# Kernel optimization log

Hardware: AMD Instinct MI355X
Metric: run time of the kernel (lower is better)

The kernel has to match this reference:

```python
import jax, jax.numpy as jnp
import numpy as np

B, L, D_MODEL, N_HEADS, M = 1, 2048, 512, 8, 128
D_HEAD = D_MODEL // N_HEADS
KERNEL_EPS = 1e-4
DENOM_EPS = 1e-6


def setup_inputs() -> dict:
    key = jax.random.key(0)
    ks = jax.random.split(key, 12)
    s = 0.02  # weight init scale
    return {
        "query": jax.random.normal(ks[0], (B, L, D_MODEL), jnp.float32),
        "key": jax.random.normal(ks[1], (B, L, D_MODEL), jnp.float32),
        "value": jax.random.normal(ks[2], (B, L, D_MODEL), jnp.float32),
        "Wq": jax.random.normal(ks[3], (D_MODEL, D_MODEL), jnp.float32) * s,
        "bq": jnp.zeros((D_MODEL,), jnp.float32),
        "Wk": jax.random.normal(ks[4], (D_MODEL, D_MODEL), jnp.float32) * s,
        "bk": jnp.zeros((D_MODEL,), jnp.float32),
        "Wv": jax.random.normal(ks[5], (D_MODEL, D_MODEL), jnp.float32) * s,
        "bv": jnp.zeros((D_MODEL,), jnp.float32),
        "Wo": jax.random.normal(ks[6], (D_MODEL, D_MODEL), jnp.float32) * s,
        "bo": jnp.zeros((D_MODEL,), jnp.float32),
        # FAVOR+ random feature matrix (d_head, m); treated as a fixed buffer
        "random_features": jax.random.normal(ks[7], (D_HEAD, M), jnp.float32),
    }


def reference(query, key, value, Wq, bq, Wk, bk, Wv, bv, Wo, bo, random_features):
    b, l, _ = query.shape

    def proj_split(x, W, bias):
        # nn.Linear: x @ W.T + b, then split heads -> (b, h, l, d_head)
        y = x @ W.T + bias
        return y.reshape(b, l, N_HEADS, D_HEAD).transpose(0, 2, 1, 3)

    q = proj_split(query, Wq, bq)
    k = proj_split(key, Wk, bk)
    v = proj_split(value, Wv, bv)

    # --- get_projected_queries_and_keys ('exp' kernel) ---
    scale = D_MODEL ** -0.25
    q = q * scale
    k = k * scale
    proj_q = q @ random_features  # (b, h, l, m)
    proj_k = k @ random_features
    h_q = -0.5 * jnp.sum(q * q, axis=-1, keepdims=True)  # (b, h, l, 1)
    h_k = -0.5 * jnp.sum(k * k, axis=-1, keepdims=True)
    # argmax over a size-1 last dim -> stabilizer is h_q itself (faithful to source)
    q_stab = h_q
    k_stab = jnp.max(h_k)  # global max, scalar
    nc = M ** -0.5
    q_prime = nc * (jnp.exp(h_q + (proj_q - q_stab)) + KERNEL_EPS)  # (b, h, l, m)
    k_prime = nc * (jnp.exp(h_k + (proj_k - k_stab)) + KERNEL_EPS)

    # --- causal numerator: per-head cumsum of k' (x) v outer products ---
    head_outs = []
    for h in range(N_HEADS):
        outer = jnp.einsum('blm,bld->blmd', k_prime[:, h], v[:, h])  # (b, l, m, d)
        prefix = jnp.cumsum(outer, axis=1)
        head_outs.append(jnp.einsum('blmd,blm->bld', prefix, q_prime[:, h]))
    numerator = jnp.stack(head_outs, axis=1)  # (b, h, l, d)

    # --- causal denominator: q' . cumsum(k') ---
    denom = jnp.einsum('bhlm,bhlm->bhl', q_prime, jnp.cumsum(k_prime, axis=2))
    context = numerator / (denom[..., None] + DENOM_EPS)

    # unshape and output projection
    context = context.transpose(0, 2, 1, 3).reshape(b, l, D_MODEL)
    return context @ Wo.T + bo
```

## Files before the change

### kernel.cpp

```cpp
#include <hip/hip_runtime.h>
#include <math.h>


#define L       2048
#define DMODEL  512
#define NH      8
#define DH      64
#define M       128
#define CT      64
#define NC      (L/CT)
#define KEPS    1e-4f
#define DEPS    1e-6f
#define SCALE   0.2102241038134286f
#define NCONST  0.08838834764831845f

#define OFF_VB     0
#define OFF_QPB    524288
#define OFF_KPB    1572864
#define OFF_SSB    2621440
#define OFF_SSZ    3670016
#define OFF_CTX    3702784
#define OFF_END    4227072

typedef short bf16x8 __attribute__((ext_vector_type(8)));
typedef float f32x4  __attribute__((ext_vector_type(4)));
typedef __bf16 bf2_t __attribute__((ext_vector_type(2)));
typedef unsigned short ushort_t;

__device__ __forceinline__ ushort_t f2bf(float f) {
    union { __bf16 b; ushort_t u; } cv;
    cv.b = (__bf16)f;
    return cv.u;
}
__device__ __forceinline__ float bf2f(ushort_t u) {
    return __uint_as_float(((unsigned)u) << 16);
}
__device__ __forceinline__ unsigned pack2(float a, float b) {
    bf2_t v;
    v.x = (__bf16)a;
    v.y = (__bf16)b;
    union { bf2_t v; unsigned u; } cv;
    cv.v = v;
    return cv.u;
}

__global__ __launch_bounds__(256) void qkvp_kernel(
    const float* __restrict__ xq, const float* __restrict__ xk, const float* __restrict__ xv,
    const float* __restrict__ Wq, const float* __restrict__ bq,
    const float* __restrict__ Wk, const float* __restrict__ bk,
    const float* __restrict__ Wv, const float* __restrict__ bv,
    const float* __restrict__ RF,
    ushort_t* __restrict__ Vb, ushort_t* __restrict__ QPb, ushort_t* __restrict__ KPb)
{
    __shared__ __align__(16) char smem[24832];
    __shared__ ushort_t Qt[64 * 136];
    __shared__ float ssq[128];
    uint4* As8 = (uint4*)smem;
    uint4* Bs8 = (uint4*)(smem + 520 * 16);
    ushort_t* RFTs = (ushort_t*)smem;

    const int tid  = threadIdx.x;
    const int lane = tid & 63;
    const int wave = tid >> 6;
    const int quad = lane >> 4;
    const int l15  = lane & 15;
    const int z = blockIdx.z;
    const int isK = (z == 1);
    const int row0 = blockIdx.x * 64;
    const int col0 = blockIdx.y * 128;

    const float* X; const float* W; const float* bias;
    if (z == 0)      { X = xq; W = Wq; bias = bq; }
    else if (z == 1) { X = xk; W = Wk; bias = bk; }
    else             { X = xv; W = Wv; bias = bv; }

    f32x4 acc[4][2];
    const f32x4 z4 = {0.f, 0.f, 0.f, 0.f};
    #pragma unroll
    for (int i = 0; i < 4; ++i) { acc[i][0] = z4; acc[i][1] = z4; }

    uint4 ra[2], rb[4];
    auto loadA = [&](int ck) {
        #pragma unroll
        for (int it = 0; it < 2; ++it) {
            int t = tid + it * 256;
            int row = t >> 3, k8 = t & 7;
            const float4* gp = (const float4*)&X[(row0 + row) * DMODEL + ck * 64 + k8 * 8];
            float4 v0 = gp[0], v1 = gp[1];
            ra[it] = make_uint4(pack2(v0.x, v0.y), pack2(v0.z, v0.w),
                                pack2(v1.x, v1.y), pack2(v1.z, v1.w));
        }
    };
    auto loadB = [&](int ck) {
        #pragma unroll
        for (int it = 0; it < 4; ++it) {
            int t = tid + it * 256;
            int col = t >> 3, k8 = t & 7;
            const float4* gp = (const float4*)&W[(col0 + col) * DMODEL + ck * 64 + k8 * 8];
            float4 v0 = gp[0], v1 = gp[1];
            rb[it] = make_uint4(pack2(v0.x, v0.y), pack2(v0.z, v0.w),
                                pack2(v1.x, v1.y), pack2(v1.z, v1.w));
        }
    };

    loadA(0); loadB(0);
    const int wn = wave;
    for (int ck = 0; ck < 8; ++ck) {
        __syncthreads();
        #pragma unroll
        for (int it = 0; it < 2; ++it) {
            int t = tid + it * 256;
            As8[(t & 7) * 65 + (t >> 3)] = ra[it];
        }
        #pragma unroll
        for (int it = 0; it < 4; ++it) {
            int t = tid + it * 256;
            Bs8[(t & 7) * 129 + (t >> 3)] = rb[it];
        }
        __syncthreads();
        if (ck < 7) { loadA(ck + 1); loadB(ck + 1); }
        const bf16x8* Av = (const bf16x8*)As8;
        const bf16x8* Bv = (const bf16x8*)Bs8;
        #pragma unroll
        for (int kc = 0; kc < 2; ++kc) {
            const int k8 = kc * 4 + quad;
            bf16x8 af[4], bfr[2];
            #pragma unroll
            for (int i = 0; i < 4; ++i) af[i] = Av[k8 * 65 + i * 16 + l15];
            #pragma unroll
            for (int j = 0; j < 2; ++j) bfr[j] = Bv[k8 * 129 + wn * 32 + j * 16 + l15];
            #pragma unroll
            for (int i = 0; i < 4; ++i)
                #pragma unroll
                for (int j = 0; j < 2; ++j)
                    acc[i][j] = __builtin_amdgcn_mfma_f32_16x16x32_bf16(af[i], bfr[j], acc[i][j], 0, 0, 0);
        }
    }

    if (z == 2) {
        #pragma unroll
        for (int i = 0; i < 4; ++i)
            #pragma unroll
            for (int j = 0; j < 2; ++j) {
                int c = col0 + wn * 32 + j * 16 + l15;
                float bv_ = bias[c];
                #pragma unroll
                for (int reg = 0; reg < 4; ++reg) {
                    int r = row0 + i * 16 + quad * 4 + reg;
                    Vb[r * DMODEL + c] = f2bf(acc[i][j][reg] + bv_);
                }
            }
        return;
    }

    #pragma unroll
    for (int i = 0; i < 4; ++i)
        #pragma unroll
        for (int j = 0; j < 2; ++j) {
            int c = wn * 32 + j * 16 + l15;
            float bv_ = bias[col0 + c];
            #pragma unroll
            for (int reg = 0; reg < 4; ++reg) {
                int r = i * 16 + quad * 4 + reg;
                Qt[r * 136 + c] = f2bf(acc[i][j][reg] + bv_);
            }
        }
    __syncthreads();

    {
        int m = tid & 127, half = tid >> 7;
        #pragma unroll
        for (int j = 0; j < 32; ++j) {
            int d = half * 32 + j;
            RFTs[m * 72 + d] = f2bf(SCALE * RF[d * M + m]);
        }
    }
    if (isK && tid < 128) {
        int hh = tid >> 6, row = tid & 63;
        float s = 0.f;
        #pragma unroll
        for (int d = 0; d < DH; ++d) {
            float v = bf2f(Qt[row * 136 + hh * 64 + d]);
            s += v * v;
        }
        ssq[tid] = s;
    }
    __syncthreads();

    const int hh = wave >> 1, mh = wave & 1;
    const float s2h = 0.5f * SCALE * SCALE;
    f32x4 pac[4][4];
    #pragma unroll
    for (int i = 0; i < 4; ++i)
        #pragma unroll
        for (int j = 0; j < 4; ++j) pac[i][j] = z4;
    #pragma unroll
    for (int kc = 0; kc < 2; ++kc) {
        bf16x8 af[4], bfr[4];
        #pragma unroll
        for (int i = 0; i < 4; ++i)
            af[i] = *(const bf16x8*)&Qt[(i * 16 + l15) * 136 + hh * 64 + kc * 32 + quad * 8];
        #pragma unroll
        for (int j = 0; j < 4; ++j)
            bfr[j] = *(const bf16x8*)&RFTs[(mh * 64 + j * 16 + l15) * 72 + kc * 32 + quad * 8];
        #pragma unroll
        for (int i = 0; i < 4; ++i)
            #pragma unroll
            for (int j = 0; j < 4; ++j)
                pac[i][j] = __builtin_amdgcn_mfma_f32_16x16x32_bf16(af[i], bfr[j], pac[i][j], 0, 0, 0);
    }

    ushort_t* dst = isK ? KPb : QPb;
    const int hgl = blockIdx.y * 2 + hh;
    #pragma unroll
    for (int i = 0; i < 4; ++i)
        #pragma unroll
        for (int reg = 0; reg < 4; ++reg) {
            int row = i * 16 + quad * 4 + reg;
            float off = isK ? (-s2h * ssq[hh * 64 + row]) : 0.f;
            #pragma unroll
            for (int j = 0; j < 4; ++j) {
                int m = mh * 64 + j * 16 + l15;
                float p = pac[i][j][reg] + off;
                dst[((long)hgl * L + row0 + row) * M + m] = f2bf(NCONST * (__expf(p) + KEPS));
            }
        }
}

__global__ __launch_bounds__(256) void out_gemm_kernel(
    const ushort_t* __restrict__ ctxb, const float* __restrict__ Wo,
    const float* __restrict__ bo, float* __restrict__ out)
{
    __shared__ uint4 As8[8 * 33];
    __shared__ uint4 Bs8[8 * 129];
    const int tid  = threadIdx.x;
    const int lane = tid & 63;
    const int wn   = tid >> 6;
    const int quad = lane >> 4;
    const int l15  = lane & 15;
    const int row0 = blockIdx.x * 32;
    const int col0 = blockIdx.y * 128;

    f32x4 acc[2][2];
    const f32x4 z4 = {0.f, 0.f, 0.f, 0.f};
    acc[0][0] = z4; acc[0][1] = z4; acc[1][0] = z4; acc[1][1] = z4;

    uint4 ra, rb[4];
    auto loadA = [&](int ck) {
        int row = tid >> 3, k8 = tid & 7;
        ra = *(const uint4*)&ctxb[(row0 + row) * DMODEL + ck * 64 + k8 * 8];
    };
    auto loadB = [&](int ck) {
        #pragma unroll
        for (int it = 0; it < 4; ++it) {
            int t = tid + it * 256;
            int col = t >> 3, k8 = t & 7;
            const float4* gp = (const float4*)&Wo[(col0 + col) * DMODEL + ck * 64 + k8 * 8];
            float4 v0 = gp[0], v1 = gp[1];
            rb[it] = make_uint4(pack2(v0.x, v0.y), pack2(v0.z, v0.w),
                                pack2(v1.x, v1.y), pack2(v1.z, v1.w));
        }
    };

    loadA(0); loadB(0);
    for (int ck = 0; ck < 8; ++ck) {
        __syncthreads();
        As8[(tid & 7) * 33 + (tid >> 3)] = ra;
        #pragma unroll
        for (int it = 0; it < 4; ++it) {
            int t = tid + it * 256;
            Bs8[(t & 7) * 129 + (t >> 3)] = rb[it];
        }
        __syncthreads();
        if (ck < 7) { loadA(ck + 1); loadB(ck + 1); }
        const bf16x8* Av = (const bf16x8*)As8;
        const bf16x8* Bv = (const bf16x8*)Bs8;
        #pragma unroll
        for (int kc = 0; kc < 2; ++kc) {
            const int k8 = kc * 4 + quad;
            bf16x8 af[2], bfr[2];
            af[0] = Av[k8 * 33 + l15];
            af[1] = Av[k8 * 33 + 16 + l15];
            #pragma unroll
            for (int j = 0; j < 2; ++j) bfr[j] = Bv[k8 * 129 + wn * 32 + j * 16 + l15];
            #pragma unroll
            for (int i = 0; i < 2; ++i)
                #pragma unroll
                for (int j = 0; j < 2; ++j)
                    acc[i][j] = __builtin_amdgcn_mfma_f32_16x16x32_bf16(af[i], bfr[j], acc[i][j], 0, 0, 0);
        }
    }
    #pragma unroll
    for (int i = 0; i < 2; ++i)
        #pragma unroll
        for (int j = 0; j < 2; ++j) {
            int c = col0 + wn * 32 + j * 16 + l15;
            float bv_ = bo[c];
            #pragma unroll
            for (int reg = 0; reg < 4; ++reg) {
                int r = row0 + i * 16 + quad * 4 + reg;
                out[r * DMODEL + c] = acc[i][j][reg] + bv_;
            }
        }
}

__global__ __launch_bounds__(256) void chunksum_mfma_kernel(
    const ushort_t* __restrict__ KPb, const ushort_t* __restrict__ Vb,
    ushort_t* __restrict__ SSb, float* __restrict__ SSz)
{
    __shared__ ushort_t Kt[128 * 72];
    __shared__ ushort_t Vt[80 * 72];
    const int tid = threadIdx.x;
    const int c = blockIdx.x, h = blockIdx.y;
    const int lane = tid & 63;
    const int wave = tid >> 6;
    const int quad = lane >> 4, l15 = lane & 15;
    const int t = lane, g = wave;

    {
        const ushort_t* kr = &KPb[((long)(h * L) + c * CT + t) * M];
        #pragma unroll
        for (int it = 0; it < 4; ++it) {
            int mo = it * 4 + g;
            uint4 u = *(const uint4*)&kr[mo * 8];
            ushort_t e[8] = {(ushort_t)(u.x & 0xffff), (ushort_t)(u.x >> 16),
                             (ushort_t)(u.y & 0xffff), (ushort_t)(u.y >> 16),
                             (ushort_t)(u.z & 0xffff), (ushort_t)(u.z >> 16),
                             (ushort_t)(u.w & 0xffff), (ushort_t)(u.w >> 16)};
            #pragma unroll
            for (int j = 0; j < 8; ++j) Kt[(mo * 8 + j) * 72 + t] = e[j];
        }
        const ushort_t* vr = &Vb[(c * CT + t) * DMODEL + h * DH];
        #pragma unroll
        for (int it = 0; it < 2; ++it) {
            int dd = it * 4 + g;
            uint4 u = *(const uint4*)&vr[dd * 8];
            ushort_t e[8] = {(ushort_t)(u.x & 0xffff), (ushort_t)(u.x >> 16),
                             (ushort_t)(u.y & 0xffff), (ushort_t)(u.y >> 16),
                             (ushort_t)(u.z & 0xffff), (ushort_t)(u.z >> 16),
                             (ushort_t)(u.w & 0xffff), (ushort_t)(u.w >> 16)};
            #pragma unroll
            for (int j = 0; j < 8; ++j) Vt[(dd * 8 + j) * 72 + t] = e[j];
        }
        if (g == 0) Vt[64 * 72 + t] = 0x3F80;
        if (g == 1) {
            #pragma unroll
            for (int r = 65; r < 80; ++r) Vt[r * 72 + t] = 0;
        }
    }
    __syncthreads();

    f32x4 acc[2][5];
    const f32x4 z4 = {0.f, 0.f, 0.f, 0.f};
    #pragma unroll
    for (int i = 0; i < 2; ++i)
        #pragma unroll
        for (int j = 0; j < 5; ++j) acc[i][j] = z4;
    #pragma unroll
    for (int kt = 0; kt < 2; ++kt) {
        bf16x8 af[2], bfr[5];
        #pragma unroll
        for (int i = 0; i < 2; ++i)
            af[i] = *(const bf16x8*)&Kt[(wave * 32 + i * 16 + l15) * 72 + kt * 32 + quad * 8];
        #pragma unroll
        for (int j = 0; j < 5; ++j)
            bfr[j] = *(const bf16x8*)&Vt[(j * 16 + l15) * 72 + kt * 32 + quad * 8];
        #pragma unroll
        for (int i = 0; i < 2; ++i)
            #pragma unroll
            for (int j = 0; j < 5; ++j)
                acc[i][j] = __builtin_amdgcn_mfma_f32_16x16x32_bf16(af[i], bfr[j], acc[i][j], 0, 0, 0);
    }
    ushort_t* outS = SSb + (long)(h * NC + c) * 8192;
    #pragma unroll
    for (int i = 0; i < 2; ++i)
        #pragma unroll
        for (int reg = 0; reg < 4; ++reg) {
            int m = wave * 32 + i * 16 + quad * 4 + reg;
            #pragma unroll
            for (int j = 0; j < 4; ++j)
                outS[m * 64 + j * 16 + l15] = f2bf(acc[i][j][reg]);
            if (l15 == 0) SSz[(h * NC + c) * M + m] = acc[i][4][reg];
        }
}

__global__ __launch_bounds__(256) void prefix_kernel(
    ushort_t* __restrict__ SSb, float* __restrict__ SSz)
{
    const int h = blockIdx.y;
    if (blockIdx.x == 32) {
        const int m = threadIdx.x;
        if (m < M) {
            float v[NC];
            #pragma unroll
            for (int c = 0; c < NC; ++c) v[c] = SSz[(h * NC + c) * M + m];
            float run = 0.f;
            #pragma unroll
            for (int c = 0; c < NC; ++c) {
                SSz[(h * NC + c) * M + m] = run;
                run += v[c];
            }
        }
        return;
    }
    const int idx = blockIdx.x * 256 + threadIdx.x;
    ushort_t v[NC];
    #pragma unroll
    for (int c = 0; c < NC; ++c) v[c] = SSb[(long)(h * NC + c) * 8192 + idx];
    float run = 0.f;
    #pragma unroll
    for (int c = 0; c < NC; ++c) {
        SSb[(long)(h * NC + c) * 8192 + idx] = f2bf(run);
        run += bf2f(v[c]);
    }
}

__global__ __launch_bounds__(512) void attn_kernel(
    const ushort_t* __restrict__ QPb, const ushort_t* __restrict__ KPb,
    const ushort_t* __restrict__ Vb, const ushort_t* __restrict__ SSb,
    const float* __restrict__ SSz, ushort_t* __restrict__ ctxb)
{
    __shared__ ushort_t Qp[64 * 136];
    __shared__ ushort_t Kp[64 * 136];
    __shared__ ushort_t St[80 * 136];
    __shared__ ushort_t Vt[80 * 72];
    __shared__ ushort_t Am[64 * 72];
    __shared__ float den[CT];
    const int tid = threadIdx.x;
    const int c = blockIdx.x, h = blockIdx.y;
    const int lane = tid & 63;
    const int wave = tid >> 6;
    const int i  = wave & 3;
    const int nh = wave >> 2;
    const int quad = lane >> 4;
    const int l15  = lane & 15;

    for (int t = tid; t < 2048; t += 512) {
        int mat = t >> 10, r = (t >> 4) & 63, c8 = t & 15;
        const ushort_t* src = mat ? KPb : QPb;
        uint4 u = *(const uint4*)&src[((long)(h * L) + c * CT + r) * M + c8 * 8];
        ushort_t* dst = mat ? Kp : Qp;
        *(uint4*)&dst[r * 136 + c8 * 8] = u;
    }
    {
        int t = tid & 63, dg = tid >> 6;
        uint4 u = *(const uint4*)&Vb[(c * CT + t) * DMODEL + h * DH + dg * 8];
        ushort_t e[8] = {(ushort_t)(u.x & 0xffff), (ushort_t)(u.x >> 16),
                         (ushort_t)(u.y & 0xffff), (ushort_t)(u.y >> 16),
                         (ushort_t)(u.z & 0xffff), (ushort_t)(u.z >> 16),
                         (ushort_t)(u.w & 0xffff), (ushort_t)(u.w >> 16)};
        #pragma unroll
        for (int j = 0; j < 8; ++j) Vt[(dg * 8 + j) * 72 + t] = e[j];
    }
    {
        const ushort_t* ssb = SSb + (long)(h * NC + c) * 8192;
        int m = tid & 127, dg = tid >> 7;
        #pragma unroll
        for (int it = 0; it < 2; ++it) {
            int dd = it * 4 + dg;
            uint4 u = *(const uint4*)&ssb[m * 64 + dd * 8];
            ushort_t e[8] = {(ushort_t)(u.x & 0xffff), (ushort_t)(u.x >> 16),
                             (ushort_t)(u.y & 0xffff), (ushort_t)(u.y >> 16),
                             (ushort_t)(u.z & 0xffff), (ushort_t)(u.z >> 16),
                             (ushort_t)(u.w & 0xffff), (ushort_t)(u.w >> 16)};
            #pragma unroll
            for (int j = 0; j < 8; ++j) St[(dd * 8 + j) * 136 + m] = e[j];
        }
    }
    if (tid < 128) St[64 * 136 + tid] = f2bf(SSz[(h * NC + c) * M + tid]);
    if (tid >= 128 && tid < 192) Vt[64 * 72 + (tid - 128)] = 0x3F80;
    for (int t = tid; t < 15 * 136; t += 512) St[65 * 136 + t] = 0;
    for (int t = tid; t < 15 * 72; t += 512)  Vt[65 * 72 + t] = 0;
    __syncthreads();

    f32x4 acc1[2];
    const f32x4 z4 = {0.f, 0.f, 0.f, 0.f};
    acc1[0] = z4; acc1[1] = z4;
    #pragma unroll
    for (int kt = 0; kt < 4; ++kt) {
        bf16x8 af = *(const bf16x8*)&Qp[(i * 16 + l15) * 136 + kt * 32 + quad * 8];
        #pragma unroll
        for (int jt = 0; jt < 2; ++jt) {
            bf16x8 bf = *(const bf16x8*)&Kp[(nh * 32 + jt * 16 + l15) * 136 + kt * 32 + quad * 8];
            acc1[jt] = __builtin_amdgcn_mfma_f32_16x16x32_bf16(af, bf, acc1[jt], 0, 0, 0);
        }
    }
    #pragma unroll
    for (int jt = 0; jt < 2; ++jt) {
        int col = nh * 32 + jt * 16 + l15;
        #pragma unroll
        for (int reg = 0; reg < 4; ++reg) {
            int row = i * 16 + quad * 4 + reg;
            Am[row * 72 + col] = f2bf((col <= row) ? acc1[jt][reg] : 0.f);
        }
    }
    __syncthreads();

    f32x4 acc2[2], acc3;
    acc2[0] = z4; acc2[1] = z4; acc3 = z4;
    #pragma unroll
    for (int kt = 0; kt < 6; ++kt) {
        bf16x8 af = (kt < 2)
            ? *(const bf16x8*)&Am[(i * 16 + l15) * 72 + kt * 32 + quad * 8]
            : *(const bf16x8*)&Qp[(i * 16 + l15) * 136 + (kt - 2) * 32 + quad * 8];
        #pragma unroll
        for (int jt = 0; jt < 2; ++jt) {
            int n = nh * 32 + jt * 16 + l15;
            bf16x8 bf = (kt < 2)
                ? *(const bf16x8*)&Vt[n * 72 + kt * 32 + quad * 8]
                : *(const bf16x8*)&St[n * 136 + (kt - 2) * 32 + quad * 8];
            acc2[jt] = __builtin_amdgcn_mfma_f32_16x16x32_bf16(af, bf, acc2[jt], 0, 0, 0);
        }
        if (nh == 0) {
            bf16x8 bz = (kt < 2)
                ? *(const bf16x8*)&Vt[(64 + l15) * 72 + kt * 32 + quad * 8]
                : *(const bf16x8*)&St[(64 + l15) * 136 + (kt - 2) * 32 + quad * 8];
            acc3 = __builtin_amdgcn_mfma_f32_16x16x32_bf16(af, bz, acc3, 0, 0, 0);
        }
    }
    if (nh == 0 && l15 == 0) {
        #pragma unroll
        for (int reg = 0; reg < 4; ++reg)
            den[i * 16 + quad * 4 + reg] = acc3[reg];
    }
    __syncthreads();
    #pragma unroll
    for (int jt = 0; jt < 2; ++jt) {
        int d = nh * 32 + jt * 16 + l15;
        #pragma unroll
        for (int reg = 0; reg < 4; ++reg) {
            int row = i * 16 + quad * 4 + reg;
            ctxb[(c * CT + row) * DMODEL + h * DH + d] = f2bf(acc2[jt][reg] / (den[row] + DEPS));
        }
    }
}

extern "C" void kernel_launch(void* const* d_in, const int* in_sizes, int n_in,
                              void* d_out, int out_size, void* d_ws, size_t ws_size,
                              hipStream_t stream)
{
    const float* query = (const float*)d_in[0];
    const float* key_  = (const float*)d_in[1];
    const float* value = (const float*)d_in[2];
    const float* Wq = (const float*)d_in[3];
    const float* bq = (const float*)d_in[4];
    const float* Wk = (const float*)d_in[5];
    const float* bk = (const float*)d_in[6];
    const float* Wv = (const float*)d_in[7];
    const float* bv = (const float*)d_in[8];
    const float* Wo = (const float*)d_in[9];
    const float* bo = (const float*)d_in[10];
    const float* RF = (const float*)d_in[11];

    float* ws = (float*)d_ws;
    ushort_t* Vb   = (ushort_t*)(ws + OFF_VB);
    ushort_t* QPb  = (ushort_t*)(ws + OFF_QPB);
    ushort_t* KPb  = (ushort_t*)(ws + OFF_KPB);
    ushort_t* SSb  = (ushort_t*)(ws + OFF_SSB);
    float* SSz     = ws + OFF_SSZ;
    ushort_t* CTXB = (ushort_t*)(ws + OFF_CTX);

    qkvp_kernel<<<dim3(32, 4, 3), 256, 0, stream>>>(query, key_, value,
                                                    Wq, bq, Wk, bk, Wv, bv, RF,
                                                    Vb, QPb, KPb);
    chunksum_mfma_kernel<<<dim3(NC, 8), 256, 0, stream>>>(KPb, Vb, SSb, SSz);
    prefix_kernel<<<dim3(33, 8), 256, 0, stream>>>(SSb, SSz);
    attn_kernel<<<dim3(NC, 8), 512, 0, stream>>>(QPb, KPb, Vb, SSb, SSz, CTXB);
    out_gemm_kernel<<<dim3(64, 4), 256, 0, stream>>>(CTXB, Wo, bo, (float*)d_out);
}
```

Before: 118.9 us.

## Fuse chunksum, prefix, attention and output GEMM into one persistent kernel with grid barriers

Replaces four separate kernel launches (chunk sums, prefix scan, intra-chunk attention, output projection) with a single 256-block persistent kernel that separates the phases with atomic-counter grid barriers. The barrier counters are reset by the preceding QKV projection kernel. V tiles stay in shared memory from the chunk-sum phase into the attention phase instead of being reloaded. The intent is to remove launch gaps and tail effects between small dependent kernels. The risks are spin-wait overhead, a deadlock if the 256 blocks of 512 threads with about 77KB of shared memory cannot all be resident at once, and the larger 512-thread block layout used for the chunk-sum and GEMM phases.

```diff
diff --git a/kernel.cpp b/kernel.cpp
--- a/kernel.cpp
+++ b/kernel.cpp
@@ -13,6 +13,7 @@
 #define DEPS    1e-6f
 #define SCALE   0.2102241038134286f
 #define NCONST  0.08838834764831845f
+#define NBLK    256
 
 #define OFF_VB     0
 #define OFF_QPB    524288
@@ -20,7 +21,8 @@
 #define OFF_SSB    2621440
 #define OFF_SSZ    3670016
 #define OFF_CTX    3702784
-#define OFF_END    4227072
+#define OFF_BAR    4227072
+#define OFF_END    4227076
 
 typedef short bf16x8 __attribute__((ext_vector_type(8)));
 typedef float f32x4  __attribute__((ext_vector_type(4)));
@@ -43,6 +45,24 @@
     cv.v = v;
     return cv.u;
 }
+__device__ __forceinline__ void unpack8(uint4 u, ushort_t* e) {
+    e[0] = (ushort_t)(u.x & 0xffff); e[1] = (ushort_t)(u.x >> 16);
+    e[2] = (ushort_t)(u.y & 0xffff); e[3] = (ushort_t)(u.y >> 16);
+    e[4] = (ushort_t)(u.z & 0xffff); e[5] = (ushort_t)(u.z >> 16);
+    e[6] = (ushort_t)(u.w & 0xffff); e[7] = (ushort_t)(u.w >> 16);
+}
+
+__device__ __forceinline__ void grid_barrier(unsigned* bar) {
+    __syncthreads();
+    if (threadIdx.x == 0) {
+        __threadfence();
+        __hip_atomic_fetch_add(bar, 1u, __ATOMIC_ACQ_REL, __HIP_MEMORY_SCOPE_AGENT);
+        while (__hip_atomic_load(bar, __ATOMIC_RELAXED, __HIP_MEMORY_SCOPE_AGENT) < (unsigned)NBLK)
+            __builtin_amdgcn_s_sleep(2);
+        __threadfence();
+    }
+    __syncthreads();
+}
 
 __global__ __launch_bounds__(256) void qkvp_kernel(
     const float* __restrict__ xq, const float* __restrict__ xk, const float* __restrict__ xv,
@@ -50,7 +70,8 @@
     const float* __restrict__ Wk, const float* __restrict__ bk,
     const float* __restrict__ Wv, const float* __restrict__ bv,
     const float* __restrict__ RF,
-    ushort_t* __restrict__ Vb, ushort_t* __restrict__ QPb, ushort_t* __restrict__ KPb)
+    ushort_t* __restrict__ Vb, ushort_t* __restrict__ QPb, ushort_t* __restrict__ KPb,
+    unsigned* __restrict__ bar)
 {
     __shared__ __align__(16) char smem[24832];
     __shared__ ushort_t Qt[64 * 136];
@@ -58,6 +79,9 @@
     uint4* As8 = (uint4*)smem;
     uint4* Bs8 = (uint4*)(smem + 520 * 16);
     ushort_t* RFTs = (ushort_t*)smem;
+
+    if (blockIdx.x == 0 && blockIdx.y == 0 && blockIdx.z == 0 && threadIdx.x < 4)
+        bar[threadIdx.x] = 0u;
 
     const int tid  = threadIdx.x;
     const int lane = tid & 63;
@@ -227,310 +251,257 @@
         }
 }
 
-__global__ __launch_bounds__(256) void out_gemm_kernel(
-    const ushort_t* __restrict__ ctxb, const float* __restrict__ Wo,
-    const float* __restrict__ bo, float* __restrict__ out)
+__global__ __launch_bounds__(512) void mega_kernel(
+    const ushort_t* __restrict__ QPb, const ushort_t* __restrict__ KPb,
+    const ushort_t* __restrict__ Vb,
+    ushort_t* __restrict__ SSb, float* __restrict__ SSz,
+    ushort_t* __restrict__ ctxb,
+    const float* __restrict__ Wo, const float* __restrict__ bo,
+    float* __restrict__ out, unsigned* __restrict__ bar)
 {
-    __shared__ uint4 As8[8 * 33];
-    __shared__ uint4 Bs8[8 * 129];
+    __shared__ __align__(16) char SM[77568];
+    ushort_t* Vt = (ushort_t*)(SM);
+    ushort_t* Qp = (ushort_t*)(SM + 11520);
+    ushort_t* Kp = (ushort_t*)(SM + 28928);
+    ushort_t* St = (ushort_t*)(SM + 46336);
+    ushort_t* Am = (ushort_t*)(SM + 68096);
+    float*    den = (float*)(SM + 77312);
+    ushort_t* Kt = (ushort_t*)(SM + 11520);
+
     const int tid  = threadIdx.x;
     const int lane = tid & 63;
-    const int wn   = tid >> 6;
+    const int wave = tid >> 6;
     const int quad = lane >> 4;
     const int l15  = lane & 15;
-    const int row0 = blockIdx.x * 32;
-    const int col0 = blockIdx.y * 128;
-
-    f32x4 acc[2][2];
+    const int bid  = blockIdx.x;
+    const int c = bid & 31, h = bid >> 5;
     const f32x4 z4 = {0.f, 0.f, 0.f, 0.f};
-    acc[0][0] = z4; acc[0][1] = z4; acc[1][0] = z4; acc[1][1] = z4;
-
-    uint4 ra, rb[4];
-    auto loadA = [&](int ck) {
-        int row = tid >> 3, k8 = tid & 7;
-        ra = *(const uint4*)&ctxb[(row0 + row) * DMODEL + ck * 64 + k8 * 8];
-    };
-    auto loadB = [&](int ck) {
-        #pragma unroll
-        for (int it = 0; it < 4; ++it) {
-            int t = tid + it * 256;
-            int col = t >> 3, k8 = t & 7;
-            const float4* gp = (const float4*)&Wo[(col0 + col) * DMODEL + ck * 64 + k8 * 8];
-            float4 v0 = gp[0], v1 = gp[1];
-            rb[it] = make_uint4(pack2(v0.x, v0.y), pack2(v0.z, v0.w),
-                                pack2(v1.x, v1.y), pack2(v1.z, v1.w));
-        }
-    };
-
-    loadA(0); loadB(0);
-    for (int ck = 0; ck < 8; ++ck) {
+
+    {
+        const ushort_t* kr = &KPb[((long)(h * L) + c * CT + lane) * M];
+        #pragma unroll
+        for (int it = 0; it < 2; ++it) {
+            int mo = it * 8 + wave;
+            uint4 u = *(const uint4*)&kr[mo * 8];
+            ushort_t e[8]; unpack8(u, e);
+            #pragma unroll
+            for (int j = 0; j < 8; ++j) Kt[(mo * 8 + j) * 72 + lane] = e[j];
+        }
+        const ushort_t* vr = &Vb[(c * CT + lane) * DMODEL + h * DH];
+        {
+            int dd = wave;
+            uint4 u = *(const uint4*)&vr[dd * 8];
+            ushort_t e[8]; unpack8(u, e);
+            #pragma unroll
+            for (int j = 0; j < 8; ++j) Vt[(dd * 8 + j) * 72 + lane] = e[j];
+        }
+        if (wave == 0) Vt[64 * 72 + lane] = 0x3F80;
+        if (wave == 1) {
+            #pragma unroll
+            for (int r = 65; r < 80; ++r) Vt[r * 72 + lane] = 0;
+        }
         __syncthreads();
-        As8[(tid & 7) * 33 + (tid >> 3)] = ra;
-        #pragma unroll
-        for (int it = 0; it < 4; ++it) {
-            int t = tid + it * 256;
-            Bs8[(t & 7) * 129 + (t >> 3)] = rb[it];
-        }
+
+        f32x4 acc[5];
+        #pragma unroll
+        for (int j = 0; j < 5; ++j) acc[j] = z4;
+        #pragma unroll
+        for (int kt = 0; kt < 2; ++kt) {
+            bf16x8 af = *(const bf16x8*)&Kt[(wave * 16 + l15) * 72 + kt * 32 + quad * 8];
+            #pragma unroll
+            for (int j = 0; j < 5; ++j) {
+                bf16x8 bfr = *(const bf16x8*)&Vt[(j * 16 + l15) * 72 + kt * 32 + quad * 8];
+                acc[j] = __builtin_amdgcn_mfma_f32_16x16x32_bf16(af, bfr, acc[j], 0, 0, 0);
+            }
+        }
+        ushort_t* outS = SSb + (long)(h * NC + c) * 8192;
+        #pragma unroll
+        for (int reg = 0; reg < 4; ++reg) {
+            int m = wave * 16 + quad * 4 + reg;
+            #pragma unroll
+            for (int j = 0; j < 4; ++j)
+                outS[m * 64 + j * 16 + l15] = f2bf(acc[j][reg]);
+            if (l15 == 0) SSz[(h * NC + c) * M + m] = acc[4][reg];
+        }
+    }
+    grid_barrier(bar + 0);
+
+    {
+        if (tid < 256) {
+            const int idx = c * 256 + tid;
+            const long base = (long)h * NC * 8192 + idx;
+            ushort_t v[NC];
+            #pragma unroll
+            for (int cc = 0; cc < NC; ++cc) v[cc] = SSb[base + (long)cc * 8192];
+            float run = 0.f;
+            #pragma unroll
+            for (int cc = 0; cc < NC; ++cc) {
+                SSb[base + (long)cc * 8192] = f2bf(run);
+                run += bf2f(v[cc]);
+            }
+        } else if (c == 0 && tid < 384) {
+            const int m = tid - 256;
+            float v[NC];
+            #pragma unroll
+            for (int cc = 0; cc < NC; ++cc) v[cc] = SSz[(h * NC + cc) * M + m];
+            float run = 0.f;
+            #pragma unroll
+            for (int cc = 0; cc < NC; ++cc) {
+                SSz[(h * NC + cc) * M + m] = run;
+                run += v[cc];
+            }
+        }
+    }
+    grid_barrier(bar + 1);
+
+    {
+        const int iw = wave & 3;
+        const int nh = wave >> 2;
+
+        for (int t = tid; t < 2048; t += 512) {
+            int mat = t >> 10, r = (t >> 4) & 63, c8 = t & 15;
+            const ushort_t* src = mat ? KPb : QPb;
+            uint4 u = *(const uint4*)&src[((long)(h * L) + c * CT + r) * M + c8 * 8];
+            ushort_t* dst = mat ? Kp : Qp;
+            *(uint4*)&dst[r * 136 + c8 * 8] = u;
+        }
+        {
+            const ushort_t* ssb = SSb + (long)(h * NC + c) * 8192;
+            int m = tid & 127, dg = tid >> 7;
+            #pragma unroll
+            for (int it = 0; it < 2; ++it) {
+                int dd = it * 4 + dg;
+                uint4 u = *(const uint4*)&ssb[m * 64 + dd * 8];
+                ushort_t e[8]; unpack8(u, e);
+                #pragma unroll
+                for (int j = 0; j < 8; ++j) St[(dd * 8 + j) * 136 + m] = e[j];
+            }
+        }
+        if (tid < 128) St[64 * 136 + tid] = f2bf(SSz[(h * NC + c) * M + tid]);
+        for (int t = tid; t < 15 * 136; t += 512) St[65 * 136 + t] = 0;
         __syncthreads();
-        if (ck < 7) { loadA(ck + 1); loadB(ck + 1); }
-        const bf16x8* Av = (const bf16x8*)As8;
-        const bf16x8* Bv = (const bf16x8*)Bs8;
-        #pragma unroll
-        for (int kc = 0; kc < 2; ++kc) {
-            const int k8 = kc * 4 + quad;
-            bf16x8 af[2], bfr[2];
-            af[0] = Av[k8 * 33 + l15];
-            af[1] = Av[k8 * 33 + 16 + l15];
-            #pragma unroll
-            for (int j = 0; j < 2; ++j) bfr[j] = Bv[k8 * 129 + wn * 32 + j * 16 + l15];
-            #pragma unroll
-            for (int i = 0; i < 2; ++i)
-                #pragma unroll
-                for (int j = 0; j < 2; ++j)
-                    acc[i][j] = __builtin_amdgcn_mfma_f32_16x16x32_bf16(af[i], bfr[j], acc[i][j], 0, 0, 0);
-        }
-    }
-    #pragma unroll
-    for (int i = 0; i < 2; ++i)
+
+        f32x4 acc1[2];
+        acc1[0] = z4; acc1[1] = z4;
+        #pragma unroll
+        for (int kt = 0; kt < 4; ++kt) {
+            bf16x8 af = *(const bf16x8*)&Qp[(iw * 16 + l15) * 136 + kt * 32 + quad * 8];
+            #pragma unroll
+            for (int jt = 0; jt < 2; ++jt) {
+                bf16x8 bf = *(const bf16x8*)&Kp[(nh * 32 + jt * 16 + l15) * 136 + kt * 32 + quad * 8];
+                acc1[jt] = __builtin_amdgcn_mfma_f32_16x16x32_bf16(af, bf, acc1[jt], 0, 0, 0);
+            }
+        }
+        #pragma unroll
+        for (int jt = 0; jt < 2; ++jt) {
+            int col = nh * 32 + jt * 16 + l15;
+            #pragma unroll
+            for (int reg = 0; reg < 4; ++reg) {
+                int row = iw * 16 + quad * 4 + reg;
+                Am[row * 72 + col] = f2bf((col <= row) ? acc1[jt][reg] : 0.f);
+            }
+        }
+        __syncthreads();
+
+        f32x4 acc2[2], acc3;
+        acc2[0] = z4; acc2[1] = z4; acc3 = z4;
+        #pragma unroll
+        for (int kt = 0; kt < 6; ++kt) {
+            bf16x8 af = (kt < 2)
+                ? *(const bf16x8*)&Am[(iw * 16 + l15) * 72 + kt * 32 + quad * 8]
+                : *(const bf16x8*)&Qp[(iw * 16 + l15) * 136 + (kt - 2) * 32 + quad * 8];
+            #pragma unroll
+            for (int jt = 0; jt < 2; ++jt) {
+                int n = nh * 32 + jt * 16 + l15;
+                bf16x8 bf = (kt < 2)
+                    ? *(const bf16x8*)&Vt[n * 72 + kt * 32 + quad * 8]
+                    : *(const bf16x8*)&St[n * 136 + (kt - 2) * 32 + quad * 8];
+                acc2[jt] = __builtin_amdgcn_mfma_f32_16x16x32_bf16(af, bf, acc2[jt], 0, 0, 0);
+            }
+            if (nh == 0) {
+                bf16x8 bz = (kt < 2)
+                    ? *(const bf16x8*)&Vt[(64 + l15) * 72 + kt * 32 + quad * 8]
+                    : *(const bf16x8*)&St[(64 + l15) * 136 + (kt - 2) * 32 + quad * 8];
+                acc3 = __builtin_amdgcn_mfma_f32_16x16x32_bf16(af, bz, acc3, 0, 0, 0);
+            }
+        }
+        if (nh == 0 && l15 == 0) {
+            #pragma unroll
+            for (int reg = 0; reg < 4; ++reg)
+                den[iw * 16 + quad * 4 + reg] = acc3[reg];
+        }
+        __syncthreads();
+        #pragma unroll
+        for (int jt = 0; jt < 2; ++jt) {
+            int d = nh * 32 + jt * 16 + l15;
+            #pragma unroll
+            for (int reg = 0; reg < 4; ++reg) {
+                int row = iw * 16 + quad * 4 + reg;
+                ctxb[(c * CT + row) * DMODEL + h * DH + d] = f2bf(acc2[jt][reg] / (den[row] + DEPS));
+            }
+        }
+    }
+    grid_barrier(bar + 2);
+
+    {
+        const int ro = bid & 63, co = bid >> 6;
+        const int row0 = ro * 32, col0 = co * 128;
+        uint4* As8 = (uint4*)SM;
+        uint4* Bs8 = (uint4*)(SM + 4224);
+        const int wn = wave & 3, rh = wave >> 2;
+
+        f32x4 acc[2]; acc[0] = z4; acc[1] = z4;
+        uint4 ra, rb[2];
+        auto loadA2 = [&](int ck) {
+            if (tid < 256) {
+                int row = tid >> 3, k8 = tid & 7;
+                ra = *(const uint4*)&ctxb[(row0 + row) * DMODEL + ck * 64 + k8 * 8];
+            }
+        };
+        auto loadB2 = [&](int ck) {
+            #pragma unroll
+            for (int it = 0; it < 2; ++it) {
+                int bt = tid + it * 512;
+                int col = bt >> 3, k8 = bt & 7;
+                const float4* gp = (const float4*)&Wo[(col0 + col) * DMODEL + ck * 64 + k8 * 8];
+                float4 v0 = gp[0], v1 = gp[1];
+                rb[it] = make_uint4(pack2(v0.x, v0.y), pack2(v0.z, v0.w),
+                                    pack2(v1.x, v1.y), pack2(v1.z, v1.w));
+            }
+        };
+
+        loadA2(0); loadB2(0);
+        for (int ck = 0; ck < 8; ++ck) {
+            __syncthreads();
+            if (tid < 256) As8[(tid & 7) * 33 + (tid >> 3)] = ra;
+            #pragma unroll
+            for (int it = 0; it < 2; ++it) {
+                int bt = tid + it * 512;
+                Bs8[(bt & 7) * 129 + (bt >> 3)] = rb[it];
+            }
+            __syncthreads();
+            if (ck < 7) { loadA2(ck + 1); loadB2(ck + 1); }
+            const bf16x8* Av = (const bf16x8*)As8;
+            const bf16x8* Bv = (const bf16x8*)Bs8;
+            #pragma unroll
+            for (int kc = 0; kc < 2; ++kc) {
+                const int k8 = kc * 4 + quad;
+                bf16x8 af = Av[k8 * 33 + rh * 16 + l15];
+                bf16x8 b0 = Bv[k8 * 129 + wn * 32 + l15];
+                bf16x8 b1 = Bv[k8 * 129 + wn * 32 + 16 + l15];
+                acc[0] = __builtin_amdgcn_mfma_f32_16x16x32_bf16(af, b0, acc[0], 0, 0, 0);
+                acc[1] = __builtin_amdgcn_mfma_f32_16x16x32_bf16(af, b1, acc[1], 0, 0, 0);
+            }
+        }
         #pragma unroll
         for (int j = 0; j < 2; ++j) {
-            int c = col0 + wn * 32 + j * 16 + l15;
-            float bv_ = bo[c];
+            int cc = col0 + wn * 32 + j * 16 + l15;
+            float bv_ = bo[cc];
             #pragma unroll
             for (int reg = 0; reg < 4; ++reg) {
-                int r = row0 + i * 16 + quad * 4 + reg;
-                out[r * DMODEL + c] = acc[i][j][reg] + bv_;
-            }
-        }
-}
-
-__global__ __launch_bounds__(256) void chunksum_mfma_kernel(
-    const ushort_t* __restrict__ KPb, const ushort_t* __restrict__ Vb,
-    ushort_t* __restrict__ SSb, float* __restrict__ SSz)
-{
-    __shared__ ushort_t Kt[128 * 72];
-    __shared__ ushort_t Vt[80 * 72];
-    const int tid = threadIdx.x;
-    const int c = blockIdx.x, h = blockIdx.y;
-    const int lane = tid & 63;
-    const int wave = tid >> 6;
-    const int quad = lane >> 4, l15 = lane & 15;
-    const int t = lane, g = wave;
-
-    {
-        const ushort_t* kr = &KPb[((long)(h * L) + c * CT + t) * M];
-        #pragma unroll
-        for (int it = 0; it < 4; ++it) {
-            int mo = it * 4 + g;
-            uint4 u = *(const uint4*)&kr[mo * 8];
-            ushort_t e[8] = {(ushort_t)(u.x & 0xffff), (ushort_t)(u.x >> 16),
-                             (ushort_t)(u.y & 0xffff), (ushort_t)(u.y >> 16),
-                             (ushort_t)(u.z & 0xffff), (ushort_t)(u.z >> 16),
-                             (ushort_t)(u.w & 0xffff), (ushort_t)(u.w >> 16)};
-            #pragma unroll
-            for (int j = 0; j < 8; ++j) Kt[(mo * 8 + j) * 72 + t] = e[j];
-        }
-        const ushort_t* vr = &Vb[(c * CT + t) * DMODEL + h * DH];
-        #pragma unroll
-        for (int it = 0; it < 2; ++it) {
-            int dd = it * 4 + g;
-            uint4 u = *(const uint4*)&vr[dd * 8];
-            ushort_t e[8] = {(ushort_t)(u.x & 0xffff), (ushort_t)(u.x >> 16),
-                             (ushort_t)(u.y & 0xffff), (ushort_t)(u.y >> 16),
-                             (ushort_t)(u.z & 0xffff), (ushort_t)(u.z >> 16),
-                             (ushort_t)(u.w & 0xffff), (ushort_t)(u.w >> 16)};
-            #pragma unroll
-            for (int j = 0; j < 8; ++j) Vt[(dd * 8 + j) * 72 + t] = e[j];
-        }
-        if (g == 0) Vt[64 * 72 + t] = 0x3F80;
-        if (g == 1) {
-            #pragma unroll
-            for (int r = 65; r < 80; ++r) Vt[r * 72 + t] = 0;
-        }
-    }
-    __syncthreads();
-
-    f32x4 acc[2][5];
-    const f32x4 z4 = {0.f, 0.f, 0.f, 0.f};
-    #pragma unroll
-    for (int i = 0; i < 2; ++i)
-        #pragma unroll
-        for (int j = 0; j < 5; ++j) acc[i][j] = z4;
-    #pragma unroll
-    for (int kt = 0; kt < 2; ++kt) {
-        bf16x8 af[2], bfr[5];
-        #pragma unroll
-        for (int i = 0; i < 2; ++i)
-            af[i] = *(const bf16x8*)&Kt[(wave * 32 + i * 16 + l15) * 72 + kt * 32 + quad * 8];
-        #pragma unroll
-        for (int j = 0; j < 5; ++j)
-            bfr[j] = *(const bf16x8*)&Vt[(j * 16 + l15) * 72 + kt * 32 + quad * 8];
-        #pragma unroll
-        for (int i = 0; i < 2; ++i)
-            #pragma unroll
-            for (int j = 0; j < 5; ++j)
-                acc[i][j] = __builtin_amdgcn_mfma_f32_16x16x32_bf16(af[i], bfr[j], acc[i][j], 0, 0, 0);
-    }
-    ushort_t* outS = SSb + (long)(h * NC + c) * 8192;
-    #pragma unroll
-    for (int i = 0; i < 2; ++i)
-        #pragma unroll
-        for (int reg = 0; reg < 4; ++reg) {
-            int m = wave * 32 + i * 16 + quad * 4 + reg;
-            #pragma unroll
-            for (int j = 0; j < 4; ++j)
-                outS[m * 64 + j * 16 + l15] = f2bf(acc[i][j][reg]);
-            if (l15 == 0) SSz[(h * NC + c) * M + m] = acc[i][4][reg];
-        }
-}
-
-__global__ __launch_bounds__(256) void prefix_kernel(
-    ushort_t* __restrict__ SSb, float* __restrict__ SSz)
-{
-    const int h = blockIdx.y;
-    if (blockIdx.x == 32) {
-        const int m = threadIdx.x;
-        if (m < M) {
-            float v[NC];
-            #pragma unroll
-            for (int c = 0; c < NC; ++c) v[c] = SSz[(h * NC + c) * M + m];
-            float run = 0.f;
-            #pragma unroll
-            for (int c = 0; c < NC; ++c) {
-                SSz[(h * NC + c) * M + m] = run;
-                run += v[c];
-            }
-        }
-        return;
-    }
-    const int idx = blockIdx.x * 256 + threadIdx.x;
-    ushort_t v[NC];
-    #pragma unroll
-    for (int c = 0; c < NC; ++c) v[c] = SSb[(long)(h * NC + c) * 8192 + idx];
-    float run = 0.f;
-    #pragma unroll
-    for (int c = 0; c < NC; ++c) {
-        SSb[(long)(h * NC + c) * 8192 + idx] = f2bf(run);
-        run += bf2f(v[c]);
-    }
-}
-
-__global__ __launch_bounds__(512) void attn_kernel(
-    const ushort_t* __restrict__ QPb, const ushort_t* __restrict__ KPb,
-    const ushort_t* __restrict__ Vb, const ushort_t* __restrict__ SSb,
-    const float* __restrict__ SSz, ushort_t* __restrict__ ctxb)
-{
-    __shared__ ushort_t Qp[64 * 136];
-    __shared__ ushort_t Kp[64 * 136];
-    __shared__ ushort_t St[80 * 136];
-    __shared__ ushort_t Vt[80 * 72];
-    __shared__ ushort_t Am[64 * 72];
-    __shared__ float den[CT];
-    const int tid = threadIdx.x;
-    const int c = blockIdx.x, h = blockIdx.y;
-    const int lane = tid & 63;
-    const int wave = tid >> 6;
-    const int i  = wave & 3;
-    const int nh = wave >> 2;
-    const int quad = lane >> 4;
-    const int l15  = lane & 15;
-
-    for (int t = tid; t < 2048; t += 512) {
-        int mat = t >> 10, r = (t >> 4) & 63, c8 = t & 15;
-        const ushort_t* src = mat ? KPb : QPb;
-        uint4 u = *(const uint4*)&src[((long)(h * L) + c * CT + r) * M + c8 * 8];
-        ushort_t* dst = mat ? Kp : Qp;
-        *(uint4*)&dst[r * 136 + c8 * 8] = u;
-    }
-    {
-        int t = tid & 63, dg = tid >> 6;
-        uint4 u = *(const uint4*)&Vb[(c * CT + t) * DMODEL + h * DH + dg * 8];
-        ushort_t e[8] = {(ushort_t)(u.x & 0xffff), (ushort_t)(u.x >> 16),
-                         (ushort_t)(u.y & 0xffff), (ushort_t)(u.y >> 16),
-                         (ushort_t)(u.z & 0xffff), (ushort_t)(u.z >> 16),
-                         (ushort_t)(u.w & 0xffff), (ushort_t)(u.w >> 16)};
-        #pragma unroll
-        for (int j = 0; j < 8; ++j) Vt[(dg * 8 + j) * 72 + t] = e[j];
-    }
-    {
-        const ushort_t* ssb = SSb + (long)(h * NC + c) * 8192;
-        int m = tid & 127, dg = tid >> 7;
-        #pragma unroll
-        for (int it = 0; it < 2; ++it) {
-            int dd = it * 4 + dg;
-            uint4 u = *(const uint4*)&ssb[m * 64 + dd * 8];
-            ushort_t e[8] = {(ushort_t)(u.x & 0xffff), (ushort_t)(u.x >> 16),
-                             (ushort_t)(u.y & 0xffff), (ushort_t)(u.y >> 16),
-                             (ushort_t)(u.z & 0xffff), (ushort_t)(u.z >> 16),
-                             (ushort_t)(u.w & 0xffff), (ushort_t)(u.w >> 16)};
-            #pragma unroll
-            for (int j = 0; j < 8; ++j) St[(dd * 8 + j) * 136 + m] = e[j];
-        }
-    }
-    if (tid < 128) St[64 * 136 + tid] = f2bf(SSz[(h * NC + c) * M + tid]);
-    if (tid >= 128 && tid < 192) Vt[64 * 72 + (tid - 128)] = 0x3F80;
-    for (int t = tid; t < 15 * 136; t += 512) St[65 * 136 + t] = 0;
-    for (int t = tid; t < 15 * 72; t += 512)  Vt[65 * 72 + t] = 0;
-    __syncthreads();
-
-    f32x4 acc1[2];
-    const f32x4 z4 = {0.f, 0.f, 0.f, 0.f};
-    acc1[0] = z4; acc1[1] = z4;
-    #pragma unroll
-    for (int kt = 0; kt < 4; ++kt) {
-        bf16x8 af = *(const bf16x8*)&Qp[(i * 16 + l15) * 136 + kt * 32 + quad * 8];
-        #pragma unroll
-        for (int jt = 0; jt < 2; ++jt) {
-            bf16x8 bf = *(const bf16x8*)&Kp[(nh * 32 + jt * 16 + l15) * 136 + kt * 32 + quad * 8];
-            acc1[jt] = __builtin_amdgcn_mfma_f32_16x16x32_bf16(af, bf, acc1[jt], 0, 0, 0);
-        }
-    }
-    #pragma unroll
-    for (int jt = 0; jt < 2; ++jt) {
-        int col = nh * 32 + jt * 16 + l15;
-        #pragma unroll
-        for (int reg = 0; reg < 4; ++reg) {
-            int row = i * 16 + quad * 4 + reg;
-            Am[row * 72 + col] = f2bf((col <= row) ? acc1[jt][reg] : 0.f);
-        }
-    }
-    __syncthreads();
-
-    f32x4 acc2[2], acc3;
-    acc2[0] = z4; acc2[1] = z4; acc3 = z4;
-    #pragma unroll
-    for (int kt = 0; kt < 6; ++kt) {
-        bf16x8 af = (kt < 2)
-            ? *(const bf16x8*)&Am[(i * 16 + l15) * 72 + kt * 32 + quad * 8]
-            : *(const bf16x8*)&Qp[(i * 16 + l15) * 136 + (kt - 2) * 32 + quad * 8];
-        #pragma unroll
-        for (int jt = 0; jt < 2; ++jt) {
-            int n = nh * 32 + jt * 16 + l15;
-            bf16x8 bf = (kt < 2)
-                ? *(const bf16x8*)&Vt[n * 72 + kt * 32 + quad * 8]
-                : *(const bf16x8*)&St[n * 136 + (kt - 2) * 32 + quad * 8];
-            acc2[jt] = __builtin_amdgcn_mfma_f32_16x16x32_bf16(af, bf, acc2[jt], 0, 0, 0);
-        }
-        if (nh == 0) {
-            bf16x8 bz = (kt < 2)
-                ? *(const bf16x8*)&Vt[(64 + l15) * 72 + kt * 32 + quad * 8]
-                : *(const bf16x8*)&St[(64 + l15) * 136 + (kt - 2) * 32 + quad * 8];
-            acc3 = __builtin_amdgcn_mfma_f32_16x16x32_bf16(af, bz, acc3, 0, 0, 0);
-        }
-    }
-    if (nh == 0 && l15 == 0) {
-        #pragma unroll
-        for (int reg = 0; reg < 4; ++reg)
-            den[i * 16 + quad * 4 + reg] = acc3[reg];
-    }
-    __syncthreads();
-    #pragma unroll
-    for (int jt = 0; jt < 2; ++jt) {
-        int d = nh * 32 + jt * 16 + l15;
-        #pragma unroll
-        for (int reg = 0; reg < 4; ++reg) {
-            int row = i * 16 + quad * 4 + reg;
-            ctxb[(c * CT + row) * DMODEL + h * DH + d] = f2bf(acc2[jt][reg] / (den[row] + DEPS));
+                int r = row0 + rh * 16 + quad * 4 + reg;
+                out[r * DMODEL + cc] = acc[j][reg] + bv_;
+            }
         }
     }
 }
@@ -559,12 +530,11 @@
     ushort_t* SSb  = (ushort_t*)(ws + OFF_SSB);
     float* SSz     = ws + OFF_SSZ;
     ushort_t* CTXB = (ushort_t*)(ws + OFF_CTX);
+    unsigned* bar  = (unsigned*)(ws + OFF_BAR);
 
     qkvp_kernel<<<dim3(32, 4, 3), 256, 0, stream>>>(query, key_, value,
                                                     Wq, bq, Wk, bk, Wv, bv, RF,
-                                                    Vb, QPb, KPb);
-    chunksum_mfma_kernel<<<dim3(NC, 8), 256, 0, stream>>>(KPb, Vb, SSb, SSz);
-    prefix_kernel<<<dim3(33, 8), 256, 0, stream>>>(SSb, SSz);
-    attn_kernel<<<dim3(NC, 8), 512, 0, stream>>>(QPb, KPb, Vb, SSb, SSz, CTXB);
-    out_gemm_kernel<<<dim3(64, 4), 256, 0, stream>>>(CTXB, Wo, bo, (float*)d_out);
-}
+                                                    Vb, QPb, KPb, bar);
+    mega_kernel<<<dim3(NBLK), 512, 0, stream>>>(QPb, KPb, Vb, SSb, SSz, CTXB,
+                                                Wo, bo, (float*)d_out, bar);
+}
```

Measured after the change: 204.9 us. +72.4%, slower.
